# Performance work log

Hardware: AMD Instinct MI355X
Metric: run time of the kernel (lower is better)

## Reference

```python
import jax, jax.numpy as jnp
import numpy as np

T, H, W = 365, 256, 256
IN_SZ, HID, OUT_SZ = 2, 64, 1
H_SCALE = 0.1


def setup_inputs() -> dict:
    key = jax.random.key(0)
    ks = jax.random.split(key, 9)
    lim_ih = 1.0 / np.sqrt(HID)
    return {
        "precipitation": jax.random.uniform(ks[0], (T, H, W), dtype=jnp.float32),
        "temperature": jax.random.normal(ks[1], (T, H, W), dtype=jnp.float32),
        "weight_ih": jax.random.uniform(ks[2], (3 * HID, IN_SZ), minval=-lim_ih, maxval=lim_ih, dtype=jnp.float32),
        "weight_hh": jax.random.uniform(ks[3], (3 * HID, HID), minval=-lim_ih, maxval=lim_ih, dtype=jnp.float32),
        "bias": jax.random.uniform(ks[4], (3 * HID,), minval=-lim_ih, maxval=lim_ih, dtype=jnp.float32),
        "bias_n": jax.random.uniform(ks[5], (HID,), minval=-lim_ih, maxval=lim_ih, dtype=jnp.float32),
        "out_w": jax.random.uniform(ks[6], (OUT_SZ, HID), minval=-lim_ih, maxval=lim_ih, dtype=jnp.float32),
        "out_b": jax.random.uniform(ks[7], (OUT_SZ,), minval=-lim_ih, maxval=lim_ih, dtype=jnp.float32),
        "init_h": jax.random.normal(ks[8], (HID,), dtype=jnp.float32) * H_SCALE,
    }


def reference(precipitation, temperature, weight_ih, weight_hh, bias, bias_n, out_w, out_b, init_h):
    t, h, w = temperature.shape
    # (T, N, 2) with N = H*W grid cells treated as batch
    inputs = jnp.stack([precipitation, temperature], axis=-1).reshape(t, h * w, -1)
    h0 = jnp.broadcast_to(init_h, (h * w, init_h.shape[0]))

    def step(hidden, x_t):
        igates = x_t @ weight_ih.T + bias          # (N, 3*HID)
        hgates = hidden @ weight_hh.T              # (N, 3*HID)
        ir, iz, in_ = jnp.split(igates, 3, axis=-1)
        hr, hz, hn = jnp.split(hgates, 3, axis=-1)
        reset = jax.nn.sigmoid(ir + hr)
        update = jax.nn.sigmoid(iz + hz)
        new = jnp.tanh(in_ + reset * (hn + bias_n))
        h_next = new + update * (hidden - new)    # equinox GRUCell convention
        y = (h_next @ out_w.T + out_b)[..., 0]    # (N,)
        return h_next, y

    final_h_flat, smb_flat = jax.lax.scan(step, h0, inputs)
    smb = smb_flat.reshape(t, h, w)
    final_h = final_h_flat.reshape(h, w, -1)
    return smb, final_h
```

## Files before the change

kernel.cpp:

```cpp
#include <hip/hip_runtime.h>

#define T_STEPS 365
#define NCELLS  65536

typedef __attribute__((ext_vector_type(8))) short short8;
typedef __attribute__((ext_vector_type(4))) float f32x4;

static __device__ __forceinline__ short f2bf_rne(float x) {
    union { float f; unsigned u; } v; v.f = x;
    unsigned r = v.u + 0x7fffu + ((v.u >> 16) & 1u);
    return (short)(r >> 16);
}
static __device__ __forceinline__ float bf2f(short b) {
    union { float f; unsigned u; } v; v.u = ((unsigned)(unsigned short)b) << 16;
    return v.f;
}
static __device__ __forceinline__ float fast_rcp(float x) { return __builtin_amdgcn_rcpf(x); }

__global__ __launch_bounds__(256, 2)
void gru_mfma_kernel(const float* __restrict__ precip,
                     const float* __restrict__ temp,
                     const float* __restrict__ w_ih,
                     const float* __restrict__ w_hh,
                     const float* __restrict__ bias,
                     const float* __restrict__ bias_n,
                     const float* __restrict__ out_w,
                     const float* __restrict__ out_b,
                     const float* __restrict__ init_h,
                     float* __restrict__ out)
{
    __shared__ float hbuf[4][16][68];

    const int lane = threadIdx.x & 63;
    const int wid  = threadIdx.x >> 6;
    const int c    = lane & 15;
    const int q    = lane >> 4;
    const int base = (blockIdx.x * 4 + wid) * 16;

    short8 Bf[12][2];
#pragma unroll
    for (int jt = 0; jt < 12; ++jt)
#pragma unroll
        for (int f = 0; f < 2; ++f) {
            const float* src = w_hh + ((16 * jt + c) * 64 + 32 * f + 8 * q);
#pragma unroll
            for (int e = 0; e < 8; ++e) Bf[jt][f][e] = f2bf_rne(src[e]);
        }

    float wr0[4], wr1[4], wz0[4], wz1[4], wn0[4], wn1[4];
    float br[4], bz[4], bn_[4], bnn[4], ow[4];
#pragma unroll
    for (int j = 0; j < 4; ++j) {
        const int u = 16 * j + c;
        wr0[j] = w_ih[2 * u];       wr1[j] = w_ih[2 * u + 1];
        wz0[j] = w_ih[128 + 2 * u]; wz1[j] = w_ih[129 + 2 * u];
        wn0[j] = w_ih[256 + 2 * u]; wn1[j] = w_ih[257 + 2 * u];
        br[j]  = bias[u]; bz[j] = bias[64 + u]; bn_[j] = bias[128 + u];
        bnn[j] = bias_n[u]; ow[j] = out_w[u];
    }
    const float ob = out_b[0];

    float hC[4][4];
#pragma unroll
    for (int j = 0; j < 4; ++j) {
        const float iv = init_h[16 * j + c];
#pragma unroll
        for (int reg = 0; reg < 4; ++reg) hC[j][reg] = iv;
    }
#pragma unroll
    for (int j = 0; j < 4; ++j)
#pragma unroll
        for (int reg = 0; reg < 4; ++reg)
            hbuf[wid][4 * q + reg][16 * j + c] = hC[j][reg];

    const bool selb0 = (c & 1), selb1 = (c & 2);
    const bool do_store = (c < 4);

#pragma unroll 1
    for (int t = 0; t < T_STEPS; ++t) {
        const size_t tofs = (size_t)t * NCELLS + base;
        float pv[4], tv[4];
#pragma unroll
        for (int reg = 0; reg < 4; ++reg) {
            pv[reg] = precip[tofs + 4 * q + reg];
            tv[reg] = temp  [tofs + 4 * q + reg];
        }

        const float* row = &hbuf[wid][c][0];
        f32x4 a0 = *(const f32x4*)(row + 8 * q);
        f32x4 a1 = *(const f32x4*)(row + 8 * q + 4);
        f32x4 a2 = *(const f32x4*)(row + 32 + 8 * q);
        f32x4 a3 = *(const f32x4*)(row + 32 + 8 * q + 4);
        short8 ah0, al0, ah1, al1;
#pragma unroll
        for (int e = 0; e < 4; ++e) {
            short h0 = f2bf_rne(a0[e]); ah0[e]     = h0; al0[e]     = f2bf_rne(a0[e] - bf2f(h0));
            short h1 = f2bf_rne(a1[e]); ah0[4 + e] = h1; al0[4 + e] = f2bf_rne(a1[e] - bf2f(h1));
            short h2 = f2bf_rne(a2[e]); ah1[e]     = h2; al1[e]     = f2bf_rne(a2[e] - bf2f(h2));
            short h3 = f2bf_rne(a3[e]); ah1[4 + e] = h3; al1[4 + e] = f2bf_rne(a3[e] - bf2f(h3));
        }

        f32x4 acc[12];
#pragma unroll
        for (int jt = 0; jt < 12; ++jt) {
            f32x4 a = {0.f, 0.f, 0.f, 0.f};
            a = __builtin_amdgcn_mfma_f32_16x16x32_bf16(ah0, Bf[jt][0], a, 0, 0, 0);
            a = __builtin_amdgcn_mfma_f32_16x16x32_bf16(ah1, Bf[jt][1], a, 0, 0, 0);
            a = __builtin_amdgcn_mfma_f32_16x16x32_bf16(al0, Bf[jt][0], a, 0, 0, 0);
            a = __builtin_amdgcn_mfma_f32_16x16x32_bf16(al1, Bf[jt][1], a, 0, 0, 0);
            acc[jt] = a;
        }

        float psum[4] = {0.f, 0.f, 0.f, 0.f};
#pragma unroll
        for (int j = 0; j < 4; ++j) {
#pragma unroll
            for (int reg = 0; reg < 4; ++reg) {
                const float hr = acc[j][reg];
                const float hz = acc[4 + j][reg];
                const float hn = acc[8 + j][reg];
                const float ir = fmaf(wr0[j], pv[reg], fmaf(wr1[j], tv[reg], br[j]));
                const float iz = fmaf(wz0[j], pv[reg], fmaf(wz1[j], tv[reg], bz[j]));
                const float in_= fmaf(wn0[j], pv[reg], fmaf(wn1[j], tv[reg], bn_[j]));
                const float r  = fast_rcp(1.f + __expf(-(ir + hr)));
                const float z  = fast_rcp(1.f + __expf(-(iz + hz)));
                const float a_ = fmaf(r, hn + bnn[j], in_);
                const float th = 1.f - 2.f * fast_rcp(1.f + __expf(a_ + a_));
                const float hnew = fmaf(z, hC[j][reg] - th, th);
                hC[j][reg] = hnew;
                psum[reg] = fmaf(hnew, ow[j], psum[reg]);
            }
        }

#pragma unroll
        for (int j = 0; j < 4; ++j)
#pragma unroll
            for (int reg = 0; reg < 4; ++reg)
                hbuf[wid][4 * q + reg][16 * j + c] = hC[j][reg];

#pragma unroll
        for (int reg = 0; reg < 4; ++reg) {
            psum[reg] += __shfl_xor(psum[reg], 1);
            psum[reg] += __shfl_xor(psum[reg], 2);
            psum[reg] += __shfl_xor(psum[reg], 4);
            psum[reg] += __shfl_xor(psum[reg], 8);
        }
        float ya = selb0 ? psum[1] : psum[0];
        float yb = selb0 ? psum[3] : psum[2];
        float yv = selb1 ? yb : ya;
        if (do_store) out[tofs + 4 * q + c] = yv + ob;
    }

    const size_t fofs = (size_t)T_STEPS * NCELLS + (size_t)base * 64;
#pragma unroll
    for (int j = 0; j < 4; ++j)
#pragma unroll
        for (int reg = 0; reg < 4; ++reg)
            out[fofs + (size_t)(4 * q + reg) * 64 + 16 * j + c] = hC[j][reg];
}

extern "C" void kernel_launch(void* const* d_in, const int* in_sizes, int n_in,
                              void* d_out, int out_size, void* d_ws, size_t ws_size,
                              hipStream_t stream) {
    const float* precip = (const float*)d_in[0];
    const float* temp   = (const float*)d_in[1];
    const float* w_ih   = (const float*)d_in[2];
    const float* w_hh   = (const float*)d_in[3];
    const float* bias   = (const float*)d_in[4];
    const float* bias_n = (const float*)d_in[5];
    const float* out_w  = (const float*)d_in[6];
    const float* out_b  = (const float*)d_in[7];
    const float* init_h = (const float*)d_in[8];

    gru_mfma_kernel<<<NCELLS / 64, 256, 0, stream>>>(
        precip, temp, w_ih, w_hh, bias, bias_n, out_w, out_b, init_h,
        (float*)d_out);
}
```

Before: 2.431 ms.

## Fold input projection and biases into MFMA via split-bf16 augmented operand

Moves the per-step input-gate projections and biases (including bias_n) onto the matrix cores. Each step builds an extra A fragment from hi/lo bf16 splits of precipitation and temperature plus a constant 1.0 column. It multiplies this against a precomputed shared-memory table of split bf16 weights and biases. This removes the per-element FMA chains and about 44 weight/bias registers. In exchange it adds 16 extra MFMAs and 16 LDS loads per step, plus a __syncthreads at setup, and it slightly changes numerical precision.

```diff
diff --git a/kernel.cpp b/kernel.cpp
--- a/kernel.cpp
+++ b/kernel.cpp
@@ -16,6 +16,9 @@
     return v.f;
 }
 static __device__ __forceinline__ float fast_rcp(float x) { return __builtin_amdgcn_rcpf(x); }
+static __device__ __forceinline__ unsigned pk16(short a, short b) {
+    return (unsigned)(unsigned short)a | ((unsigned)(unsigned short)b << 16);
+}
 
 __global__ __launch_bounds__(256, 2)
 void gru_mfma_kernel(const float* __restrict__ precip,
@@ -29,7 +32,8 @@
                      const float* __restrict__ init_h,
                      float* __restrict__ out)
 {
-    __shared__ float hbuf[4][16][68];
+    __shared__ __align__(16) float hbuf[4][16][68];
+    __shared__ __align__(16) unsigned xw_u[64 + 16 * 68];
 
     const int lane = threadIdx.x & 63;
     const int wid  = threadIdx.x >> 6;
@@ -37,6 +41,31 @@
     const int q    = lane >> 4;
     const int base = (blockIdx.x * 4 + wid) * 16;
 
+    if (threadIdx.x < 64) xw_u[threadIdx.x] = 0u;
+    {
+        const int frag = threadIdx.x >> 4, cc = threadIdx.x & 15;
+        float w0 = 0.f, w1 = 0.f, b = 0.f;
+        if (frag < 8) {
+            const int u = 16 * frag + cc;
+            w0 = w_ih[2 * u]; w1 = w_ih[2 * u + 1]; b = bias[u];
+        } else if (frag < 12) {
+            const int u = 16 * (frag - 8) + cc;
+            b = bias_n[u];
+        } else {
+            const int u = 16 * (frag - 12) + cc;
+            w0 = w_ih[256 + 2 * u]; w1 = w_ih[257 + 2 * u]; b = bias[128 + u];
+        }
+        const short w0h = f2bf_rne(w0), w1h = f2bf_rne(w1);
+        const short w0l = f2bf_rne(w0 - bf2f(w0h)), w1l = f2bf_rne(w1 - bf2f(w1h));
+        const short bh  = f2bf_rne(b),  bl  = f2bf_rne(b - bf2f(bh));
+        unsigned* dst = &xw_u[64 + cc * 68 + frag * 4];
+        const unsigned wpk = pk16(w0h, w1h);
+        dst[0] = wpk;
+        dst[1] = wpk;
+        dst[2] = pk16(w0l, w1l);
+        dst[3] = pk16(bh, bl);
+    }
+
     short8 Bf[12][2];
 #pragma unroll
     for (int jt = 0; jt < 12; ++jt)
@@ -47,17 +76,9 @@
             for (int e = 0; e < 8; ++e) Bf[jt][f][e] = f2bf_rne(src[e]);
         }
 
-    float wr0[4], wr1[4], wz0[4], wz1[4], wn0[4], wn1[4];
-    float br[4], bz[4], bn_[4], bnn[4], ow[4];
-#pragma unroll
-    for (int j = 0; j < 4; ++j) {
-        const int u = 16 * j + c;
-        wr0[j] = w_ih[2 * u];       wr1[j] = w_ih[2 * u + 1];
-        wz0[j] = w_ih[128 + 2 * u]; wz1[j] = w_ih[129 + 2 * u];
-        wn0[j] = w_ih[256 + 2 * u]; wn1[j] = w_ih[257 + 2 * u];
-        br[j]  = bias[u]; bz[j] = bias[64 + u]; bn_[j] = bias[128 + u];
-        bnn[j] = bias_n[u]; ow[j] = out_w[u];
-    }
+    float ow[4];
+#pragma unroll
+    for (int j = 0; j < 4; ++j) ow[j] = out_w[16 * j + c];
     const float ob = out_b[0];
 
     float hC[4][4];
@@ -72,6 +93,10 @@
 #pragma unroll
         for (int reg = 0; reg < 4; ++reg)
             hbuf[wid][4 * q + reg][16 * j + c] = hC[j][reg];
+
+    __syncthreads();
+
+    const unsigned* xwp = xw_u + ((q == 0) ? (64 + c * 68) : 0);
 
     const bool selb0 = (c & 1), selb1 = (c & 2);
     const bool do_store = (c < 4);
@@ -79,12 +104,17 @@
 #pragma unroll 1
     for (int t = 0; t < T_STEPS; ++t) {
         const size_t tofs = (size_t)t * NCELLS + base;
-        float pv[4], tv[4];
-#pragma unroll
-        for (int reg = 0; reg < 4; ++reg) {
-            pv[reg] = precip[tofs + 4 * q + reg];
-            tv[reg] = temp  [tofs + 4 * q + reg];
-        }
+
+        const float pc = precip[tofs + c];
+        const float tc = temp  [tofs + c];
+        const short ph = f2bf_rne(pc), th_ = f2bf_rne(tc);
+        const short pl = f2bf_rne(pc - bf2f(ph)), tl = f2bf_rne(tc - bf2f(th_));
+        union { unsigned u[4]; short8 s; } ax;
+        ax.u[0] = pk16(ph, th_);
+        ax.u[1] = pk16(pl, tl);
+        ax.u[2] = ax.u[0];
+        ax.u[3] = 0x3F803F80u;
+        const short8 Ax = ax.s;
 
         const float* row = &hbuf[wid][c][0];
         f32x4 a0 = *(const f32x4*)(row + 8 * q);
@@ -100,31 +130,37 @@
             short h3 = f2bf_rne(a3[e]); ah1[4 + e] = h3; al1[4 + e] = f2bf_rne(a3[e] - bf2f(h3));
         }
 
-        f32x4 acc[12];
+        f32x4 acc[16];
 #pragma unroll
         for (int jt = 0; jt < 12; ++jt) {
+            const short8 Bx = *(const short8*)(xwp + 4 * jt);
             f32x4 a = {0.f, 0.f, 0.f, 0.f};
+            a = __builtin_amdgcn_mfma_f32_16x16x32_bf16(Ax,  Bx,        a, 0, 0, 0);
             a = __builtin_amdgcn_mfma_f32_16x16x32_bf16(ah0, Bf[jt][0], a, 0, 0, 0);
             a = __builtin_amdgcn_mfma_f32_16x16x32_bf16(ah1, Bf[jt][1], a, 0, 0, 0);
             a = __builtin_amdgcn_mfma_f32_16x16x32_bf16(al0, Bf[jt][0], a, 0, 0, 0);
             a = __builtin_amdgcn_mfma_f32_16x16x32_bf16(al1, Bf[jt][1], a, 0, 0, 0);
             acc[jt] = a;
         }
+#pragma unroll
+        for (int j2 = 0; j2 < 4; ++j2) {
+            const short8 Bx = *(const short8*)(xwp + 4 * (12 + j2));
+            f32x4 a = {0.f, 0.f, 0.f, 0.f};
+            acc[12 + j2] = __builtin_amdgcn_mfma_f32_16x16x32_bf16(Ax, Bx, a, 0, 0, 0);
+        }
 
         float psum[4] = {0.f, 0.f, 0.f, 0.f};
 #pragma unroll
         for (int j = 0; j < 4; ++j) {
 #pragma unroll
             for (int reg = 0; reg < 4; ++reg) {
-                const float hr = acc[j][reg];
-                const float hz = acc[4 + j][reg];
-                const float hn = acc[8 + j][reg];
-                const float ir = fmaf(wr0[j], pv[reg], fmaf(wr1[j], tv[reg], br[j]));
-                const float iz = fmaf(wz0[j], pv[reg], fmaf(wz1[j], tv[reg], bz[j]));
-                const float in_= fmaf(wn0[j], pv[reg], fmaf(wn1[j], tv[reg], bn_[j]));
-                const float r  = fast_rcp(1.f + __expf(-(ir + hr)));
-                const float z  = fast_rcp(1.f + __expf(-(iz + hz)));
-                const float a_ = fmaf(r, hn + bnn[j], in_);
+                const float gr = acc[j][reg];
+                const float gz = acc[4 + j][reg];
+                const float gn = acc[8 + j][reg];
+                const float gi = acc[12 + j][reg];
+                const float r  = fast_rcp(1.f + __expf(-gr));
+                const float z  = fast_rcp(1.f + __expf(-gz));
+                const float a_ = fmaf(r, gn, gi);
                 const float th = 1.f - 2.f * fast_rcp(1.f + __expf(a_ + a_));
                 const float hnew = fmaf(z, hC[j][reg] - th, th);
                 hC[j][reg] = hnew;
```

After: 2.649 ms. 1.09x slower.
